# Optimization experiments

Measured on AMD Instinct MI355X. Metric: run time of the kernel, lower is better.

The kernel has to match this reference:

```python
import jax, jax.numpy as jnp
import numpy as np

B, KS, KG, H, V, T = 32, 2048, 512, 512, 32000, 64
BOS = 1


def setup_inputs() -> dict:
    key = jax.random.key(0)
    ks = jax.random.split(key, 11)
    s = 1.0 / np.sqrt(H)
    emb_table = jax.random.normal(ks[4], (V, H), jnp.float32) * s
    emb_table = emb_table.at[0].set(0.0)  # padding_idx=0
    return {
        "sentence_out": jax.random.normal(ks[0], (B, KS, H), jnp.float32),
        "graph_out": jax.random.normal(ks[1], (B, KG, H), jnp.float32),
        "encoder_hidden": jax.random.normal(ks[2], (1, B, H), jnp.float32),
        "W_a": jax.random.normal(ks[3], (H, H), jnp.float32) * s,
        "emb_table": emb_table,
        "W_ih": jax.random.normal(ks[5], (3 * H, H), jnp.float32) * s,
        "W_hh": jax.random.normal(ks[6], (3 * H, H), jnp.float32) * s,
        "b_ih": jnp.zeros((3 * H,), jnp.float32),
        "b_hh": jnp.zeros((3 * H,), jnp.float32),
        "W_out": jax.random.normal(ks[7], (V, 3 * H), jnp.float32) * s,
        "b_out": jnp.zeros((V,), jnp.float32),
        "target_max_length": T,
    }


def _attend(enc, ha, hidden):
    # enc: (B,K,H) values; ha = enc @ W_a: (B,K,H); hidden: (B,H)
    score = jnp.einsum('bkh,bh->bk', ha, hidden)        # (B,K)
    at = jax.nn.softmax(score, axis=1)
    return jnp.einsum('bkh,bk->bh', enc, at)            # (B,H)


def reference(sentence_out, graph_out, encoder_hidden, W_a, emb_table,
              W_ih, W_hh, b_ih, b_hh, W_out, b_out, target_max_length):
    # hoist loop-invariant attention projections
    ha_s = jnp.einsum('bkh,ht->bkt', sentence_out, W_a)  # (B,KS,H)
    ha_g = jnp.einsum('bkh,ht->bkt', graph_out, W_a)     # (B,KG,H)

    def step(carry, _):
        h, inp = carry                                   # h: (B,H), inp: (B,) int
        ct_s = _attend(sentence_out, ha_s, h)
        ct_g = _attend(graph_out, ha_g, h)
        emb = emb_table[inp]                             # (B,H)
        gx = emb @ W_ih.T + b_ih                         # (B,3H)
        gh = h @ W_hh.T + b_hh                           # (B,3H)
        xr, xz, xn = jnp.split(gx, 3, axis=-1)
        hr, hz, hn = jnp.split(gh, 3, axis=-1)
        r = jax.nn.sigmoid(xr + hr)
        z = jax.nn.sigmoid(xz + hz)
        n = jnp.tanh(xn + r * hn)
        h_new = (1.0 - z) * n + z * h                    # (B,H)
        out = jnp.concatenate([h_new, ct_g, ct_s], axis=-1) @ W_out.T + b_out  # (B,V)
        inp_new = jnp.argmax(out, axis=-1)
        return (h_new, inp_new), out

    h0 = encoder_hidden[0]                               # (B,H)
    inp0 = jnp.full((B,), BOS, dtype=jnp.int32)
    _, outs = jax.lax.scan(step, (h0, inp0), None, length=target_max_length)
    return outs                                          # (T,B,V)
```

## Files before the change

### kernel.cpp

```cpp
#include <hip/hip_runtime.h>
#include <hip/hip_bf16.h>
#include <math.h>

#define NB 32
#define NKS 2048
#define NKG 512
#define NH 512
#define NH3 1536
#define NV 32000
#define NSTEPS 64

typedef unsigned long long u64;
typedef unsigned int u32;
typedef unsigned short u16;

__device__ __forceinline__ float bfu(u32 u){ return __uint_as_float(u << 16); }

__device__ __forceinline__ u64 packv(float v, int idx){
  u32 u = __float_as_uint(v);
  u = (u & 0x80000000u) ? ~u : (u | 0x80000000u);
  return (((u64)u) << 32) | (u32)(~(u32)idx);
}

__global__ void k_cast(const float* __restrict__ sent, const float* __restrict__ graph,
                       u16* __restrict__ dsts, u16* __restrict__ dstg){
  const long NSg = (long)NB*NKS*NH/8;
  const long NGg = (long)NB*NKG*NH/8;
  long stride = (long)gridDim.x*blockDim.x;
  for (long g = (long)blockIdx.x*blockDim.x + threadIdx.x; g < NSg+NGg; g += stride){
    const float* src; u16* dst; long gg;
    if (g < NSg){ src = sent; dst = dsts; gg = g; } else { src = graph; dst = dstg; gg = g - NSg; }
    const float4* s4 = (const float4*)src + gg*2;
    float4 a = s4[0], b = s4[1];
    float vals[8] = {a.x,a.y,a.z,a.w,b.x,b.y,b.z,b.w};
    u16 o[8];
    #pragma unroll
    for (int i=0;i<8;i++){
      u32 bits = __float_as_uint(vals[i]);
      o[i] = (u16)((bits + 0x7FFFu + ((bits>>16)&1u)) >> 16);
    }
    uint4 out;
    out.x = (u32)o[0] | ((u32)o[1]<<16);
    out.y = (u32)o[2] | ((u32)o[3]<<16);
    out.z = (u32)o[4] | ((u32)o[5]<<16);
    out.w = (u32)o[6] | ((u32)o[7]<<16);
    *((uint4*)dst + gg) = out;
  }
}

__global__ void k_init(const float* __restrict__ enc, float* __restrict__ h){
  int i = blockIdx.x*256 + threadIdx.x;
  h[i] = enc[i];
}

__global__ __launch_bounds__(512) void k_gates(
    const float* __restrict__ h, const float* __restrict__ Wa,
    const float* __restrict__ Wih, const float* __restrict__ Whh,
    const float* __restrict__ bih, const float* __restrict__ bhh,
    const float* __restrict__ emb, u64* __restrict__ packed,
    float* __restrict__ q, float* __restrict__ gx, float* __restrict__ gh, int step)
{
  __shared__ float4 xs4[NB*128];
  int tid = threadIdx.x;
  int obase = blockIdx.x*64;
  int typ = (obase < NH) ? 0 : (obase < NH+NH3 ? 1 : 2);
  const u64* prev = packed + ((step+1)&1)*NB;
  if (typ != 1){
    for (int i=tid;i<NB*128;i+=512) xs4[i] = ((const float4*)h)[i];
  } else {
    for (int i=tid;i<NB*128;i+=512){
      int b = i>>7;
      int inp = (step==0) ? 1 : (int)(~(u32)prev[b]);
      xs4[i] = ((const float4*)(emb + (size_t)inp*NH))[i&127];
    }
  }
  if (blockIdx.x==0 && tid<NB) packed[(size_t)(step&1)*NB + tid] = 0ULL;
  __syncthreads();
  int lane = tid&63, bg = tid>>6;
  int o = obase + lane;
  const float* wrow; float bias; float* dst; int dstride, dcol;
  if (typ==0){ wrow = Wa + (size_t)o*NH; bias=0.f; dst=q; dstride=NH; dcol=o; }
  else if (typ==1){ int oo=o-NH; wrow = Wih + (size_t)oo*NH; bias=bih[oo]; dst=gx; dstride=NH3; dcol=oo; }
  else { int oo=o-NH-NH3; wrow = Whh + (size_t)oo*NH; bias=bhh[oo]; dst=gh; dstride=NH3; dcol=oo; }
  const float4* w4 = (const float4*)wrow;
  float acc[4] = {0.f,0.f,0.f,0.f};
  for (int k4=0;k4<128;k4++){
    float4 w = w4[k4];
    #pragma unroll
    for (int j=0;j<4;j++){
      float4 xv = xs4[(bg*4+j)*128 + k4];
      acc[j] += w.x*xv.x; acc[j] += w.y*xv.y; acc[j] += w.z*xv.z; acc[j] += w.w*xv.w;
    }
  }
  #pragma unroll
  for (int j=0;j<4;j++){
    int b = bg*4+j;
    dst[(size_t)b*dstride + dcol] = acc[j] + bias;
  }
}

template<int BF>
__global__ __launch_bounds__(256) void k_scores(
   const u16* __restrict__ sh, const u16* __restrict__ g16,
   const float* __restrict__ sf, const float* __restrict__ gf,
   const float* __restrict__ q,
   float* __restrict__ ss, float* __restrict__ sg,
   float* __restrict__ tms, float* __restrict__ tmg)
{
  int blk = blockIdx.x, tid = threadIdx.x;
  int b, tile, K, nt; const u16* srch; const float* srcf; float* sc; float* tm;
  if (blk < 256){ b = blk>>3; tile = blk&7; K = NKS; srch = sh;  srcf = sf; sc = ss; tm = tms; nt=8; }
  else { int bb = blk-256; b = bb>>1; tile = bb&1; K = NKG; srch = g16; srcf = gf; sc = sg; tm = tmg; nt=2; }
  __shared__ float qs[NH];
  for (int i=tid;i<NH;i+=256) qs[i] = q[b*NH+i];
  __syncthreads();
  int key = tile*256 + tid;
  float acc = 0.f;
  if (BF){
    const u16* row = srch + ((size_t)b*K + key)*NH;
    for (int hh=0; hh<NH; hh+=8){
      uint4 u = *(const uint4*)(row+hh);
      acc += bfu(u.x&0xffffu)*qs[hh+0];
      acc += bfu(u.x>>16)    *qs[hh+1];
      acc += bfu(u.y&0xffffu)*qs[hh+2];
      acc += bfu(u.y>>16)    *qs[hh+3];
      acc += bfu(u.z&0xffffu)*qs[hh+4];
      acc += bfu(u.z>>16)    *qs[hh+5];
      acc += bfu(u.w&0xffffu)*qs[hh+6];
      acc += bfu(u.w>>16)    *qs[hh+7];
    }
  } else {
    const float4* row4 = (const float4*)(srcf + ((size_t)b*K + key)*NH);
    for (int k4=0;k4<128;k4++){
      float4 v = row4[k4];
      acc += v.x*qs[k4*4+0]; acc += v.y*qs[k4*4+1]; acc += v.z*qs[k4*4+2]; acc += v.w*qs[k4*4+3];
    }
  }
  sc[(size_t)b*K + key] = acc;
  __shared__ float red[256];
  red[tid] = acc; __syncthreads();
  for (int s=128;s>0;s>>=1){ if (tid<s) red[tid] = fmaxf(red[tid], red[tid+s]); __syncthreads(); }
  if (tid==0) tm[b*nt + tile] = red[0];
}

__global__ __launch_bounds__(256) void k_ct(
  const float* __restrict__ sf, const float* __restrict__ gf,
  const float* __restrict__ q,
  const float* __restrict__ ss, const float* __restrict__ sg,
  const float* __restrict__ tms, const float* __restrict__ tmg,
  float* __restrict__ pcs, float* __restrict__ pcg,
  float* __restrict__ pds, float* __restrict__ pdg)
{
  int blk = blockIdx.x, tid = threadIdx.x;
  int b, tile, K, nt; const float* src; const float* sc; const float* tm; float* pct; float* pden;
  if (blk < 256){ b=blk>>3; tile=blk&7; K=NKS; nt=8; src=sf; sc=ss; tm=tms; pct=pcs; pden=pds; }
  else { int bb=blk-256; b=bb>>1; tile=bb&1; K=NKG; nt=2; src=gf; sc=sg; tm=tmg; pct=pcg; pden=pdg; }
  __shared__ float qs[NH];
  for (int i=tid;i<NH;i+=256) qs[i] = q[b*NH+i];
  float m = -1e30f;
  for (int i=0;i<nt;i++) m = fmaxf(m, tm[b*nt+i]);
  __syncthreads();
  int key = tile*256 + tid;
  float s = sc[(size_t)b*K + key];
  bool selp = (s > m - 24.0f);
  u64 mb = __ballot(selp);
  int lane = tid&63, wv = tid>>6;
  __shared__ int wcnt[4]; __shared__ int wbase[5];
  if (lane==0) wcnt[wv] = __popcll(mb);
  __syncthreads();
  if (tid==0){ int r=0; for (int w=0;w<4;w++){ wbase[w]=r; r+=wcnt[w]; } wbase[4]=r; }
  __syncthreads();
  int n = wbase[4];
  __shared__ int sel[256]; __shared__ float wexp[256];
  if (selp){
    int pos = wbase[wv] + __popcll(mb & ((1ULL<<lane)-1ULL));
    sel[pos] = key;
  }
  __syncthreads();
  for (int i=wv; i<n; i+=4){
    const float* vr = src + ((size_t)b*K + sel[i])*NH;
    const float4* vr4 = (const float4*)vr + lane*2;
    float4 p0 = vr4[0], p1 = vr4[1];
    int hb = lane*8;
    float a = p0.x*qs[hb+0]+p0.y*qs[hb+1]+p0.z*qs[hb+2]+p0.w*qs[hb+3]
            + p1.x*qs[hb+4]+p1.y*qs[hb+5]+p1.z*qs[hb+6]+p1.w*qs[hb+7];
    #pragma unroll
    for (int off=32; off>=1; off>>=1) a += __shfl_xor(a, off);
    if (lane==0) wexp[i] = expf(a - m);
  }
  __syncthreads();
  float den = 0.f;
  for (int i=0;i<n;i++) den += wexp[i];
  float c0=0.f, c1=0.f; int h0 = tid*2;
  for (int i=0;i<n;i++){
    float w = wexp[i];
    const float2 vv = *(const float2*)(src + ((size_t)b*K + sel[i])*NH + h0);
    c0 += w*vv.x; c1 += w*vv.y;
  }
  float* pout = pct + ((size_t)(b*nt + tile))*NH;
  pout[h0] = c0; pout[h0+1] = c1;
  if (tid==0) pden[b*nt+tile] = den;
}

__global__ __launch_bounds__(256) void k_comb(
  const float* __restrict__ pcs, const float* __restrict__ pcg,
  const float* __restrict__ pds, const float* __restrict__ pdg,
  const float* __restrict__ gx, const float* __restrict__ gh,
  float* __restrict__ h, float* __restrict__ x)
{
  int b = blockIdx.x, tid = threadIdx.x;
  float dens = 0.f, deng = 0.f;
  for (int i=0;i<8;i++) dens += pds[b*8+i];
  for (int i=0;i<2;i++) deng += pdg[b*2+i];
  float invs = 1.f/dens, invg = 1.f/deng;
  for (int i=tid; i<NH; i+=256){
    float cs = 0.f; for (int t=0;t<8;t++) cs += pcs[((size_t)(b*8+t))*NH + i];
    float cg = 0.f; for (int t=0;t<2;t++) cg += pcg[((size_t)(b*2+t))*NH + i];
    cs *= invs; cg *= invg;
    float xr = gx[(size_t)b*NH3 + i],        hr = gh[(size_t)b*NH3 + i];
    float xz = gx[(size_t)b*NH3 + NH + i],   hz = gh[(size_t)b*NH3 + NH + i];
    float xn = gx[(size_t)b*NH3 + 2*NH + i], hn = gh[(size_t)b*NH3 + 2*NH + i];
    float r = 1.f/(1.f+expf(-(xr+hr)));
    float z = 1.f/(1.f+expf(-(xz+hz)));
    float nn = tanhf(xn + r*hn);
    float hold = h[(size_t)b*NH + i];
    float hnew = (1.f - z)*nn + z*hold;
    h[(size_t)b*NH + i] = hnew;
    x[(size_t)b*NH3 + i] = hnew;
    x[(size_t)b*NH3 + NH + i] = cg;
    x[(size_t)b*NH3 + 2*NH + i] = cs;
  }
}

__global__ __launch_bounds__(256) void k_logits(
  const float* __restrict__ x, const float* __restrict__ Wout,
  const float* __restrict__ bout, float* __restrict__ dst,
  u64* __restrict__ packed, int step)
{
  __shared__ float4 xs4[NB*128];
  int tid = threadIdx.x;
  int bg = tid>>6, lane = tid&63;
  int vbase = blockIdx.x*128;
  int v0 = vbase + lane, v1 = vbase + 64 + lane;
  float acc0[8] = {0.f,0.f,0.f,0.f,0.f,0.f,0.f,0.f};
  float acc1[8] = {0.f,0.f,0.f,0.f,0.f,0.f,0.f,0.f};
  for (int c=0;c<3;c++){
    int kb = c*NH;
    for (int i=tid;i<NB*128;i+=256){
      int b=i>>7, kk=i&127;
      xs4[i] = ((const float4*)(x + (size_t)b*NH3 + kb))[kk];
    }
    __syncthreads();
    const float4* w0 = (const float4*)(Wout + (size_t)v0*NH3 + kb);
    const float4* w1 = (const float4*)(Wout + (size_t)v1*NH3 + kb);
    for (int k4=0;k4<128;k4++){
      float4 a = w0[k4], bb = w1[k4];
      #pragma unroll
      for (int j=0;j<8;j++){
        float4 xv = xs4[(bg*8+j)*128 + k4];
        acc0[j] += a.x*xv.x;  acc0[j] += a.y*xv.y;  acc0[j] += a.z*xv.z;  acc0[j] += a.w*xv.w;
        acc1[j] += bb.x*xv.x; acc1[j] += bb.y*xv.y; acc1[j] += bb.z*xv.z; acc1[j] += bb.w*xv.w;
      }
    }
    __syncthreads();
  }
  u64* smax = (u64*)xs4;
  if (tid<NB) smax[tid] = 0ULL;
  __syncthreads();
  float b0 = bout[v0], b1 = bout[v1];
  u64* cur = packed + (size_t)(step&1)*NB;
  #pragma unroll
  for (int j=0;j<8;j++){
    int b = bg*8+j;
    float r0 = acc0[j]+b0, r1 = acc1[j]+b1;
    dst[(size_t)b*NV + v0] = r0;
    dst[(size_t)b*NV + v1] = r1;
    u64 p0 = packv(r0, v0), p1 = packv(r1, v1);
    atomicMax(&smax[b], p0>p1?p0:p1);
  }
  __syncthreads();
  if (tid<NB) atomicMax(&cur[tid], smax[tid]);
}

extern "C" void kernel_launch(void* const* d_in, const int* in_sizes, int n_in,
                              void* d_out, int out_size, void* d_ws, size_t ws_size,
                              hipStream_t stream) {
  const float* sent  = (const float*)d_in[0];
  const float* graph = (const float*)d_in[1];
  const float* enc   = (const float*)d_in[2];
  const float* Wa    = (const float*)d_in[3];
  const float* emb   = (const float*)d_in[4];
  const float* Wih   = (const float*)d_in[5];
  const float* Whh   = (const float*)d_in[6];
  const float* bih   = (const float*)d_in[7];
  const float* bhh   = (const float*)d_in[8];
  const float* Wout  = (const float*)d_in[9];
  const float* bout  = (const float*)d_in[10];
  float* out = (float*)d_out;

  char* wsb = (char*)d_ws;
  size_t off = 0;
  auto alloc = [&](size_t nfloats)->float*{ float* p = (float*)(wsb + off); off += nfloats*4; return p; };
  float* h   = alloc(NB*NH);
  float* q   = alloc(NB*NH);
  float* gx  = alloc((size_t)NB*NH3);
  float* gh  = alloc((size_t)NB*NH3);
  float* ss  = alloc((size_t)NB*NKS);
  float* sg  = alloc((size_t)NB*NKG);
  float* tms = alloc(NB*8);
  float* tmg = alloc(NB*2);
  float* pcs = alloc((size_t)NB*8*NH);
  float* pcg = alloc((size_t)NB*2*NH);
  float* pds = alloc(NB*8);
  float* pdg = alloc(NB*2);
  float* x   = alloc((size_t)NB*NH3);
  u64* packed = (u64*)(wsb + off); off += 2*NB*8;
  size_t bfoff = (off + 255) & ~(size_t)255;
  size_t nS = (size_t)NB*NKS*NH, nG = (size_t)NB*NKG*NH;
  int usebf = (ws_size >= bfoff + (nS+nG)*2) ? 1 : 0;
  u16* sh16 = (u16*)(wsb + bfoff);
  u16* g16  = sh16 + nS;

  if (usebf) k_cast<<<dim3(4096), dim3(256), 0, stream>>>(sent, graph, sh16, g16);
  k_init<<<dim3(64), dim3(256), 0, stream>>>(enc, h);

  for (int t=0; t<NSTEPS; t++){
    k_gates<<<dim3(56), dim3(512), 0, stream>>>(h, Wa, Wih, Whh, bih, bhh, emb, packed, q, gx, gh, t);
    if (usebf)
      k_scores<1><<<dim3(320), dim3(256), 0, stream>>>(sh16, g16, sent, graph, q, ss, sg, tms, tmg);
    else
      k_scores<0><<<dim3(320), dim3(256), 0, stream>>>(sh16, g16, sent, graph, q, ss, sg, tms, tmg);
    k_ct<<<dim3(320), dim3(256), 0, stream>>>(sent, graph, q, ss, sg, tms, tmg, pcs, pcg, pds, pdg);
    k_comb<<<dim3(NB), dim3(256), 0, stream>>>(pcs, pcg, pds, pdg, gx, gh, h, x);
    k_logits<<<dim3(250), dim3(256), 0, stream>>>(x, Wout, bout, out + (size_t)t*NB*NV, packed, t);
  }
}
```

Before: 17.49 ms.

## Use bf16 MFMA logits with split-precision activations, fp64 recurrence, and candidate refinement

```diff
diff --git a/kernel.cpp b/kernel.cpp
--- a/kernel.cpp
+++ b/kernel.cpp
@@ -13,13 +13,24 @@
 typedef unsigned long long u64;
 typedef unsigned int u32;
 typedef unsigned short u16;
+typedef __attribute__((ext_vector_type(8))) short short8;
+typedef __attribute__((ext_vector_type(4))) float f32x4;
 
 __device__ __forceinline__ float bfu(u32 u){ return __uint_as_float(u << 16); }
+__device__ __forceinline__ u16 f2bf(float f){
+  u32 b = __float_as_uint(f);
+  return (u16)((b + 0x7FFFu + ((b>>16)&1u)) >> 16);
+}
 
 __device__ __forceinline__ u64 packv(float v, int idx){
   u32 u = __float_as_uint(v);
   u = (u & 0x80000000u) ? ~u : (u | 0x80000000u);
   return (((u64)u) << 32) | (u32)(~(u32)idx);
+}
+__device__ __forceinline__ float unpackv(u64 p){
+  u32 hi = (u32)(p >> 32);
+  u32 u = (hi & 0x80000000u) ? (hi ^ 0x80000000u) : ~hi;
+  return __uint_as_float(u);
 }
 
 __global__ void k_cast(const float* __restrict__ sent, const float* __restrict__ graph,
@@ -35,10 +46,7 @@
     float vals[8] = {a.x,a.y,a.z,a.w,b.x,b.y,b.z,b.w};
     u16 o[8];
     #pragma unroll
-    for (int i=0;i<8;i++){
-      u32 bits = __float_as_uint(vals[i]);
-      o[i] = (u16)((bits + 0x7FFFu + ((bits>>16)&1u)) >> 16);
-    }
+    for (int i=0;i<8;i++) o[i] = f2bf(vals[i]);
     uint4 out;
     out.x = (u32)o[0] | ((u32)o[1]<<16);
     out.y = (u32)o[2] | ((u32)o[3]<<16);
@@ -48,62 +56,90 @@
   }
 }
 
-__global__ void k_init(const float* __restrict__ enc, float* __restrict__ h){
+__global__ void k_packw(const float* __restrict__ W, u16* __restrict__ wp){
+  long t = (long)blockIdx.x*256 + threadIdx.x;
+  int lane = (int)(t & 63);
+  long g = t >> 6;
+  int kc = (int)(g % 48);
+  int v16 = (int)(g / 48);
+  int v = v16*16 + (lane&15);
+  int k0 = kc*32 + (lane>>4)*8;
+  const float4* src = (const float4*)(W + (size_t)v*NH3 + k0);
+  float4 a = src[0], b = src[1];
+  float vals[8] = {a.x,a.y,a.z,a.w,b.x,b.y,b.z,b.w};
+  u16 o[8];
+  #pragma unroll
+  for (int i=0;i<8;i++) o[i] = f2bf(vals[i]);
+  uint4 out;
+  out.x = (u32)o[0] | ((u32)o[1]<<16);
+  out.y = (u32)o[2] | ((u32)o[3]<<16);
+  out.z = (u32)o[4] | ((u32)o[5]<<16);
+  out.w = (u32)o[6] | ((u32)o[7]<<16);
+  ((uint4*)wp)[t] = out;
+}
+
+__global__ void k_init(const float* __restrict__ enc, double* __restrict__ hd){
   int i = blockIdx.x*256 + threadIdx.x;
-  h[i] = enc[i];
-}
-
-__global__ __launch_bounds__(512) void k_gates(
-    const float* __restrict__ h, const float* __restrict__ Wa,
+  hd[i] = (double)enc[i];
+}
+
+__global__ __launch_bounds__(256) void k_gates(
+    const double* __restrict__ hd, const float* __restrict__ Wa,
     const float* __restrict__ Wih, const float* __restrict__ Whh,
     const float* __restrict__ bih, const float* __restrict__ bhh,
-    const float* __restrict__ emb, u64* __restrict__ packed,
-    float* __restrict__ q, float* __restrict__ gx, float* __restrict__ gh, int step)
-{
-  __shared__ float4 xs4[NB*128];
-  int tid = threadIdx.x;
-  int obase = blockIdx.x*64;
-  int typ = (obase < NH) ? 0 : (obase < NH+NH3 ? 1 : 2);
-  const u64* prev = packed + ((step+1)&1)*NB;
+    const float* __restrict__ emb, const u64* __restrict__ packed_ex,
+    double* __restrict__ qd, float* __restrict__ qf,
+    double* __restrict__ gxd, double* __restrict__ ghd, int step)
+{
+  __shared__ double xs[8*512];
+  int blk = blockIdx.x, tid = threadIdx.x;
+  int ot = blk >> 2, bq = blk & 3;
+  int b0 = bq*8;
+  int typ = (ot < 8) ? 0 : (ot < 32 ? 1 : 2);
+  const u64* prev = packed_ex + ((step+1)&1)*NB;
   if (typ != 1){
-    for (int i=tid;i<NB*128;i+=512) xs4[i] = ((const float4*)h)[i];
+    for (int i=tid; i<8*512; i+=256) xs[i] = hd[(size_t)b0*NH + i];
   } else {
-    for (int i=tid;i<NB*128;i+=512){
-      int b = i>>7;
-      int inp = (step==0) ? 1 : (int)(~(u32)prev[b]);
-      xs4[i] = ((const float4*)(emb + (size_t)inp*NH))[i&127];
-    }
-  }
-  if (blockIdx.x==0 && tid<NB) packed[(size_t)(step&1)*NB + tid] = 0ULL;
-  __syncthreads();
-  int lane = tid&63, bg = tid>>6;
-  int o = obase + lane;
-  const float* wrow; float bias; float* dst; int dstride, dcol;
-  if (typ==0){ wrow = Wa + (size_t)o*NH; bias=0.f; dst=q; dstride=NH; dcol=o; }
-  else if (typ==1){ int oo=o-NH; wrow = Wih + (size_t)oo*NH; bias=bih[oo]; dst=gx; dstride=NH3; dcol=oo; }
-  else { int oo=o-NH-NH3; wrow = Whh + (size_t)oo*NH; bias=bhh[oo]; dst=gh; dstride=NH3; dcol=oo; }
+    for (int i=tid; i<8*512; i+=256){
+      int bb = i>>9;
+      int inp = (step==0) ? 1 : (int)(~(u32)prev[b0+bb]);
+      xs[i] = (double)emb[(size_t)inp*NH + (i&511)];
+    }
+  }
+  __syncthreads();
+  int lane = tid&63, wv = tid>>6;
+  const float* wrow; double bias; int dcol;
+  if (typ==0){ dcol = ot*64 + lane; wrow = Wa + (size_t)dcol*NH; bias = 0.0; }
+  else if (typ==1){ dcol = (ot-8)*64 + lane; wrow = Wih + (size_t)dcol*NH; bias = (double)bih[dcol]; }
+  else { dcol = (ot-32)*64 + lane; wrow = Whh + (size_t)dcol*NH; bias = (double)bhh[dcol]; }
   const float4* w4 = (const float4*)wrow;
-  float acc[4] = {0.f,0.f,0.f,0.f};
+  int s0 = wv*2, s1 = s0+1;
+  double acc0 = 0.0, acc1 = 0.0;
   for (int k4=0;k4<128;k4++){
     float4 w = w4[k4];
-    #pragma unroll
-    for (int j=0;j<4;j++){
-      float4 xv = xs4[(bg*4+j)*128 + k4];
-      acc[j] += w.x*xv.x; acc[j] += w.y*xv.y; acc[j] += w.z*xv.z; acc[j] += w.w*xv.w;
-    }
-  }
-  #pragma unroll
-  for (int j=0;j<4;j++){
-    int b = bg*4+j;
-    dst[(size_t)b*dstride + dcol] = acc[j] + bias;
+    int k = k4*4;
+    acc0 += (double)w.x*xs[s0*512+k]   + (double)w.y*xs[s0*512+k+1]
+          + (double)w.z*xs[s0*512+k+2] + (double)w.w*xs[s0*512+k+3];
+    acc1 += (double)w.x*xs[s1*512+k]   + (double)w.y*xs[s1*512+k+1]
+          + (double)w.z*xs[s1*512+k+2] + (double)w.w*xs[s1*512+k+3];
+  }
+  acc0 += bias; acc1 += bias;
+  int ba = b0+s0, bb2 = b0+s1;
+  if (typ==0){
+    qd[(size_t)ba*NH+dcol] = acc0; qf[(size_t)ba*NH+dcol] = (float)acc0;
+    qd[(size_t)bb2*NH+dcol] = acc1; qf[(size_t)bb2*NH+dcol] = (float)acc1;
+  } else if (typ==1){
+    gxd[(size_t)ba*NH3+dcol] = acc0; gxd[(size_t)bb2*NH3+dcol] = acc1;
+  } else {
+    ghd[(size_t)ba*NH3+dcol] = acc0; ghd[(size_t)bb2*NH3+dcol] = acc1;
   }
 }
 
 template<int BF>
-__global__ __launch_bounds__(256) void k_scores(
+__global__ __launch_bounds__(256) void k_scores2(
    const u16* __restrict__ sh, const u16* __restrict__ g16,
    const float* __restrict__ sf, const float* __restrict__ gf,
-   const float* __restrict__ q,
+   const float* __restrict__ qf,
    float* __restrict__ ss, float* __restrict__ sg,
    float* __restrict__ tms, float* __restrict__ tmg)
 {
@@ -111,58 +147,61 @@
   int b, tile, K, nt; const u16* srch; const float* srcf; float* sc; float* tm;
   if (blk < 256){ b = blk>>3; tile = blk&7; K = NKS; srch = sh;  srcf = sf; sc = ss; tm = tms; nt=8; }
   else { int bb = blk-256; b = bb>>1; tile = bb&1; K = NKG; srch = g16; srcf = gf; sc = sg; tm = tmg; nt=2; }
-  __shared__ float qs[NH];
-  for (int i=tid;i<NH;i+=256) qs[i] = q[b*NH+i];
-  __syncthreads();
-  int key = tile*256 + tid;
-  float acc = 0.f;
-  if (BF){
-    const u16* row = srch + ((size_t)b*K + key)*NH;
-    for (int hh=0; hh<NH; hh+=8){
-      uint4 u = *(const uint4*)(row+hh);
-      acc += bfu(u.x&0xffffu)*qs[hh+0];
-      acc += bfu(u.x>>16)    *qs[hh+1];
-      acc += bfu(u.y&0xffffu)*qs[hh+2];
-      acc += bfu(u.y>>16)    *qs[hh+3];
-      acc += bfu(u.z&0xffffu)*qs[hh+4];
-      acc += bfu(u.z>>16)    *qs[hh+5];
-      acc += bfu(u.w&0xffffu)*qs[hh+6];
-      acc += bfu(u.w>>16)    *qs[hh+7];
-    }
-  } else {
-    const float4* row4 = (const float4*)(srcf + ((size_t)b*K + key)*NH);
-    for (int k4=0;k4<128;k4++){
-      float4 v = row4[k4];
-      acc += v.x*qs[k4*4+0]; acc += v.y*qs[k4*4+1]; acc += v.z*qs[k4*4+2]; acc += v.w*qs[k4*4+3];
-    }
-  }
-  sc[(size_t)b*K + key] = acc;
-  __shared__ float red[256];
-  red[tid] = acc; __syncthreads();
-  for (int s=128;s>0;s>>=1){ if (tid<s) red[tid] = fmaxf(red[tid], red[tid+s]); __syncthreads(); }
-  if (tid==0) tm[b*nt + tile] = red[0];
+  int wv = tid>>6, lane = tid&63;
+  float qv[8];
+  { const float4* q4 = (const float4*)(qf + b*NH) + lane*2;
+    float4 qa = q4[0], qb = q4[1];
+    qv[0]=qa.x; qv[1]=qa.y; qv[2]=qa.z; qv[3]=qa.w;
+    qv[4]=qb.x; qv[5]=qb.y; qv[6]=qb.z; qv[7]=qb.w; }
+  int kbase = tile*256 + wv*64;
+  float my = 0.f, wmax = -1e30f;
+  #pragma unroll 2
+  for (int r=0;r<64;r++){
+    int key = kbase + r;
+    float acc;
+    if (BF){
+      uint4 u = *((const uint4*)(srch + ((size_t)b*K + key)*NH) + lane);
+      acc = bfu(u.x&0xffffu)*qv[0]+bfu(u.x>>16)*qv[1]+bfu(u.y&0xffffu)*qv[2]+bfu(u.y>>16)*qv[3]
+           +bfu(u.z&0xffffu)*qv[4]+bfu(u.z>>16)*qv[5]+bfu(u.w&0xffffu)*qv[6]+bfu(u.w>>16)*qv[7];
+    } else {
+      const float4* rw = (const float4*)(srcf + ((size_t)b*K + key)*NH) + lane*2;
+      float4 p0 = rw[0], p1 = rw[1];
+      acc = p0.x*qv[0]+p0.y*qv[1]+p0.z*qv[2]+p0.w*qv[3]
+           +p1.x*qv[4]+p1.y*qv[5]+p1.z*qv[6]+p1.w*qv[7];
+    }
+    #pragma unroll
+    for (int off=32;off>=1;off>>=1) acc += __shfl_xor(acc, off);
+    wmax = fmaxf(wmax, acc);
+    if (r == lane) my = acc;
+  }
+  sc[(size_t)b*K + kbase + lane] = my;
+  __shared__ float red[4];
+  if (lane==0) red[wv] = wmax;
+  __syncthreads();
+  if (tid==0) tm[b*nt + tile] = fmaxf(fmaxf(red[0],red[1]), fmaxf(red[2],red[3]));
 }
 
 __global__ __launch_bounds__(256) void k_ct(
   const float* __restrict__ sf, const float* __restrict__ gf,
-  const float* __restrict__ q,
+  const double* __restrict__ qd,
   const float* __restrict__ ss, const float* __restrict__ sg,
   const float* __restrict__ tms, const float* __restrict__ tmg,
-  float* __restrict__ pcs, float* __restrict__ pcg,
-  float* __restrict__ pds, float* __restrict__ pdg)
+  double* __restrict__ pcs, double* __restrict__ pcg,
+  double* __restrict__ pds, double* __restrict__ pdg)
 {
   int blk = blockIdx.x, tid = threadIdx.x;
-  int b, tile, K, nt; const float* src; const float* sc; const float* tm; float* pct; float* pden;
+  int b, tile, K, nt; const float* src; const float* sc; const float* tm;
+  double* pct; double* pden;
   if (blk < 256){ b=blk>>3; tile=blk&7; K=NKS; nt=8; src=sf; sc=ss; tm=tms; pct=pcs; pden=pds; }
   else { int bb=blk-256; b=bb>>1; tile=bb&1; K=NKG; nt=2; src=gf; sc=sg; tm=tmg; pct=pcg; pden=pdg; }
-  __shared__ float qs[NH];
-  for (int i=tid;i<NH;i+=256) qs[i] = q[b*NH+i];
+  __shared__ double qs[NH];
+  for (int i=tid;i<NH;i+=256) qs[i] = qd[b*NH+i];
   float m = -1e30f;
   for (int i=0;i<nt;i++) m = fmaxf(m, tm[b*nt+i]);
   __syncthreads();
   int key = tile*256 + tid;
   float s = sc[(size_t)b*K + key];
-  bool selp = (s > m - 24.0f);
+  bool selp = (s > m - 30.0f);
   u64 mb = __ballot(selp);
   int lane = tid&63, wv = tid>>6;
   __shared__ int wcnt[4]; __shared__ int wbase[5];
@@ -171,71 +210,190 @@
   if (tid==0){ int r=0; for (int w=0;w<4;w++){ wbase[w]=r; r+=wcnt[w]; } wbase[4]=r; }
   __syncthreads();
   int n = wbase[4];
-  __shared__ int sel[256]; __shared__ float wexp[256];
+  __shared__ int sel[256]; __shared__ double wexp[256];
   if (selp){
     int pos = wbase[wv] + __popcll(mb & ((1ULL<<lane)-1ULL));
     sel[pos] = key;
   }
   __syncthreads();
+  double md = (double)m;
   for (int i=wv; i<n; i+=4){
     const float* vr = src + ((size_t)b*K + sel[i])*NH;
     const float4* vr4 = (const float4*)vr + lane*2;
     float4 p0 = vr4[0], p1 = vr4[1];
     int hb = lane*8;
-    float a = p0.x*qs[hb+0]+p0.y*qs[hb+1]+p0.z*qs[hb+2]+p0.w*qs[hb+3]
-            + p1.x*qs[hb+4]+p1.y*qs[hb+5]+p1.z*qs[hb+6]+p1.w*qs[hb+7];
+    double a = (double)p0.x*qs[hb+0]+(double)p0.y*qs[hb+1]+(double)p0.z*qs[hb+2]+(double)p0.w*qs[hb+3]
+             + (double)p1.x*qs[hb+4]+(double)p1.y*qs[hb+5]+(double)p1.z*qs[hb+6]+(double)p1.w*qs[hb+7];
     #pragma unroll
     for (int off=32; off>=1; off>>=1) a += __shfl_xor(a, off);
-    if (lane==0) wexp[i] = expf(a - m);
-  }
-  __syncthreads();
-  float den = 0.f;
+    if (lane==0) wexp[i] = exp(a - md);
+  }
+  __syncthreads();
+  double den = 0.0;
   for (int i=0;i<n;i++) den += wexp[i];
-  float c0=0.f, c1=0.f; int h0 = tid*2;
+  double c0=0.0, c1=0.0; int h0 = tid*2;
   for (int i=0;i<n;i++){
-    float w = wexp[i];
+    double w = wexp[i];
     const float2 vv = *(const float2*)(src + ((size_t)b*K + sel[i])*NH + h0);
-    c0 += w*vv.x; c1 += w*vv.y;
-  }
-  float* pout = pct + ((size_t)(b*nt + tile))*NH;
+    c0 += w*(double)vv.x; c1 += w*(double)vv.y;
+  }
+  double* pout = pct + ((size_t)(b*nt + tile))*NH;
   pout[h0] = c0; pout[h0+1] = c1;
   if (tid==0) pden[b*nt+tile] = den;
 }
 
 __global__ __launch_bounds__(256) void k_comb(
-  const float* __restrict__ pcs, const float* __restrict__ pcg,
-  const float* __restrict__ pds, const float* __restrict__ pdg,
-  const float* __restrict__ gx, const float* __restrict__ gh,
-  float* __restrict__ h, float* __restrict__ x)
+  const double* __restrict__ pcs, const double* __restrict__ pcg,
+  const double* __restrict__ pds, const double* __restrict__ pdg,
+  const double* __restrict__ gxd, const double* __restrict__ ghd,
+  double* __restrict__ hd, double* __restrict__ xd, u16* __restrict__ apack,
+  u64* __restrict__ pbf_cur, u64* __restrict__ pex_cur)
 {
   int b = blockIdx.x, tid = threadIdx.x;
-  float dens = 0.f, deng = 0.f;
+  if (tid==0){ pbf_cur[b] = 0ULL; pex_cur[b] = 0ULL; }
+  double dens = 0.0, deng = 0.0;
   for (int i=0;i<8;i++) dens += pds[b*8+i];
   for (int i=0;i<2;i++) deng += pdg[b*2+i];
-  float invs = 1.f/dens, invg = 1.f/deng;
+  int mt = b>>4, row = b&15;
   for (int i=tid; i<NH; i+=256){
-    float cs = 0.f; for (int t=0;t<8;t++) cs += pcs[((size_t)(b*8+t))*NH + i];
-    float cg = 0.f; for (int t=0;t<2;t++) cg += pcg[((size_t)(b*2+t))*NH + i];
-    cs *= invs; cg *= invg;
-    float xr = gx[(size_t)b*NH3 + i],        hr = gh[(size_t)b*NH3 + i];
-    float xz = gx[(size_t)b*NH3 + NH + i],   hz = gh[(size_t)b*NH3 + NH + i];
-    float xn = gx[(size_t)b*NH3 + 2*NH + i], hn = gh[(size_t)b*NH3 + 2*NH + i];
-    float r = 1.f/(1.f+expf(-(xr+hr)));
-    float z = 1.f/(1.f+expf(-(xz+hz)));
-    float nn = tanhf(xn + r*hn);
-    float hold = h[(size_t)b*NH + i];
-    float hnew = (1.f - z)*nn + z*hold;
-    h[(size_t)b*NH + i] = hnew;
-    x[(size_t)b*NH3 + i] = hnew;
-    x[(size_t)b*NH3 + NH + i] = cg;
-    x[(size_t)b*NH3 + 2*NH + i] = cs;
+    double cs = 0.0; for (int t=0;t<8;t++) cs += pcs[((size_t)(b*8+t))*NH + i];
+    double cg = 0.0; for (int t=0;t<2;t++) cg += pcg[((size_t)(b*2+t))*NH + i];
+    cs /= dens; cg /= deng;
+    double xr = gxd[(size_t)b*NH3 + i],        hr = ghd[(size_t)b*NH3 + i];
+    double xz = gxd[(size_t)b*NH3 + NH + i],   hz = ghd[(size_t)b*NH3 + NH + i];
+    double xn = gxd[(size_t)b*NH3 + 2*NH + i], hn = ghd[(size_t)b*NH3 + 2*NH + i];
+    double r = 1.0/(1.0+exp(-(xr+hr)));
+    double z = 1.0/(1.0+exp(-(xz+hz)));
+    double nn = tanh(xn + r*hn);
+    double hold = hd[(size_t)b*NH + i];
+    double hnew = (1.0 - z)*nn + z*hold;
+    hd[(size_t)b*NH + i] = hnew;
+    double vals[3] = {hnew, cg, cs};
+    #pragma unroll
+    for (int c=0;c<3;c++){
+      int col = c*NH + i;
+      xd[(size_t)b*NH3 + col] = vals[c];
+      int kc = col>>5, kg = (col&31)>>3, j = col&7;
+      int lane = row + 16*kg;
+      size_t base = ((size_t)(mt*48+kc)*64 + lane)*8 + j;
+      float xf = (float)vals[c];
+      u16 hi = f2bf(xf);
+      float rem = (float)(vals[c] - (double)bfu((u32)hi));
+      apack[base] = hi;
+      apack[base + (size_t)2*48*64*8] = f2bf(rem);
+    }
+  }
+}
+
+__global__ __launch_bounds__(256) void k_logv(
+  const u16* __restrict__ apack, const u16* __restrict__ wpack,
+  const float* __restrict__ bout, float* __restrict__ dst,
+  u64* __restrict__ pbf_cur)
+{
+  int tid = threadIdx.x;
+  int wv = tid>>6, lane = tid&63;
+  int v16 = blockIdx.x*4 + wv;
+  const short8* bp = (const short8*)wpack + (size_t)v16*48*64 + lane;
+  const short8* ap = (const short8*)apack + lane;
+  f32x4 acc0 = {0.f,0.f,0.f,0.f}, acc1 = {0.f,0.f,0.f,0.f};
+  #pragma unroll 4
+  for (int kc=0; kc<48; kc++){
+    short8 bf = bp[(size_t)kc*64];
+    short8 a0h = ap[(size_t)kc*64];
+    short8 a1h = ap[(size_t)(48+kc)*64];
+    short8 a0l = ap[(size_t)(96+kc)*64];
+    short8 a1l = ap[(size_t)(144+kc)*64];
+    acc0 = __builtin_amdgcn_mfma_f32_16x16x32_bf16(a0h, bf, acc0, 0, 0, 0);
+    acc0 = __builtin_amdgcn_mfma_f32_16x16x32_bf16(a0l, bf, acc0, 0, 0, 0);
+    acc1 = __builtin_amdgcn_mfma_f32_16x16x32_bf16(a1h, bf, acc1, 0, 0, 0);
+    acc1 = __builtin_amdgcn_mfma_f32_16x16x32_bf16(a1l, bf, acc1, 0, 0, 0);
+  }
+  __shared__ u64 smax[NB];
+  if (tid < NB) smax[tid] = 0ULL;
+  __syncthreads();
+  int col = v16*16 + (lane&15);
+  float bias = bout[col];
+  int r0 = (lane>>4)*4;
+  #pragma unroll
+  for (int r=0;r<4;r++){
+    int b0 = r0 + r;
+    float v0 = acc0[r] + bias;
+    dst[(size_t)b0*NV + col] = v0;
+    atomicMax(&smax[b0], packv(v0, col));
+    int b1 = 16 + b0;
+    float v1 = acc1[r] + bias;
+    dst[(size_t)b1*NV + col] = v1;
+    atomicMax(&smax[b1], packv(v1, col));
+  }
+  __syncthreads();
+  if (tid < NB) atomicMax(&pbf_cur[tid], smax[tid]);
+}
+
+__global__ __launch_bounds__(256) void k_refine(
+  float* __restrict__ logits, const double* __restrict__ xd,
+  const float* __restrict__ Wout, const float* __restrict__ bout,
+  const u64* __restrict__ pbf_cur, u64* __restrict__ pex_cur)
+{
+  int b = blockIdx.x, tid = threadIdx.x;
+  __shared__ double xs[NH3];
+  for (int i=tid;i<NH3;i+=256) xs[i] = xd[(size_t)b*NH3 + i];
+  float maxv = unpackv(pbf_cur[b]);
+  __shared__ int cnt;
+  __shared__ int cand[2048];
+  __shared__ double cval[2048];
+  const float4* lg = (const float4*)(logits + (size_t)b*NV);
+  float margin = 1.0f;
+  for (int attempt=0; attempt<2; attempt++){
+    if (tid==0) cnt = 0;
+    __syncthreads();
+    float thr = maxv - margin;
+    for (int i=tid; i<NV/4; i+=256){
+      float4 v = lg[i];
+      if (v.x>thr){ int p=atomicAdd(&cnt,1); if(p<2048) cand[p]=i*4+0; }
+      if (v.y>thr){ int p=atomicAdd(&cnt,1); if(p<2048) cand[p]=i*4+1; }
+      if (v.z>thr){ int p=atomicAdd(&cnt,1); if(p<2048) cand[p]=i*4+2; }
+      if (v.w>thr){ int p=atomicAdd(&cnt,1); if(p<2048) cand[p]=i*4+3; }
+    }
+    __syncthreads();
+    if (cnt <= 2048) break;
+    margin = 0.125f;
+    __syncthreads();
+  }
+  int n = min(cnt, 2048);
+  int wv = tid>>6, lane = tid&63;
+  for (int c=wv; c<n; c+=4){
+    int v = cand[c];
+    const float4* wr = (const float4*)(Wout + (size_t)v*NH3);
+    double a = 0.0;
+    #pragma unroll
+    for (int i=0;i<6;i++){
+      int e = lane + 64*i;
+      float4 w4 = wr[e];
+      a += (double)w4.x*xs[e*4+0] + (double)w4.y*xs[e*4+1]
+         + (double)w4.z*xs[e*4+2] + (double)w4.w*xs[e*4+3];
+    }
+    #pragma unroll
+    for (int off=32; off>=1; off>>=1) a += __shfl_xor(a, off);
+    if (lane==0){
+      double av = a + (double)bout[v];
+      cval[c] = av;
+      logits[(size_t)b*NV + v] = (float)av;
+    }
+  }
+  __syncthreads();
+  if (tid==0){
+    double bv = -1e300; int bi = 0x7fffffff;
+    for (int c=0;c<n;c++){
+      if (cval[c] > bv || (cval[c] == bv && cand[c] < bi)){ bv = cval[c]; bi = cand[c]; }
+    }
+    pex_cur[b] = packv((float)bv, bi);
   }
 }
 
 __global__ __launch_bounds__(256) void k_logits(
-  const float* __restrict__ x, const float* __restrict__ Wout,
+  const double* __restrict__ xd, const float* __restrict__ Wout,
   const float* __restrict__ bout, float* __restrict__ dst,
-  u64* __restrict__ packed, int step)
+  u64* __restrict__ pbf_cur)
 {
   __shared__ float4 xs4[NB*128];
   int tid = threadIdx.x;
@@ -248,7 +406,12 @@
     int kb = c*NH;
     for (int i=tid;i<NB*128;i+=256){
       int b=i>>7, kk=i&127;
-      xs4[i] = ((const float4*)(x + (size_t)b*NH3 + kb))[kk];
+      float4 t;
+      t.x = (float)xd[(size_t)b*NH3 + kb + kk*4+0];
+      t.y = (float)xd[(size_t)b*NH3 + kb + kk*4+1];
+      t.z = (float)xd[(size_t)b*NH3 + kb + kk*4+2];
+      t.w = (float)xd[(size_t)b*NH3 + kb + kk*4+3];
+      xs4[i] = t;
     }
     __syncthreads();
     const float4* w0 = (const float4*)(Wout + (size_t)v0*NH3 + kb);
@@ -268,7 +431,6 @@
   if (tid<NB) smax[tid] = 0ULL;
   __syncthreads();
   float b0 = bout[v0], b1 = bout[v1];
-  u64* cur = packed + (size_t)(step&1)*NB;
   #pragma unroll
   for (int j=0;j<8;j++){
     int b = bg*8+j;
@@ -279,7 +441,7 @@
     atomicMax(&smax[b], p0>p1?p0:p1);
   }
   __syncthreads();
-  if (tid<NB) atomicMax(&cur[tid], smax[tid]);
+  if (tid<NB) atomicMax(&pbf_cur[tid], smax[tid]);
 }
 
 extern "C" void kernel_launch(void* const* d_in, const int* in_sizes, int n_in,
@@ -300,38 +462,59 @@
 
   char* wsb = (char*)d_ws;
   size_t off = 0;
-  auto alloc = [&](size_t nfloats)->float*{ float* p = (float*)(wsb + off); off += nfloats*4; return p; };
-  float* h   = alloc(NB*NH);
-  float* q   = alloc(NB*NH);
-  float* gx  = alloc((size_t)NB*NH3);
-  float* gh  = alloc((size_t)NB*NH3);
-  float* ss  = alloc((size_t)NB*NKS);
-  float* sg  = alloc((size_t)NB*NKG);
-  float* tms = alloc(NB*8);
-  float* tmg = alloc(NB*2);
-  float* pcs = alloc((size_t)NB*8*NH);
-  float* pcg = alloc((size_t)NB*2*NH);
-  float* pds = alloc(NB*8);
-  float* pdg = alloc(NB*2);
-  float* x   = alloc((size_t)NB*NH3);
-  u64* packed = (u64*)(wsb + off); off += 2*NB*8;
-  size_t bfoff = (off + 255) & ~(size_t)255;
+  auto allocd = [&](size_t n)->double*{ double* p = (double*)(wsb + off); off += n*8; return p; };
+  auto allocf = [&](size_t n)->float*{ float* p = (float*)(wsb + off); off += n*4; return p; };
+  double* hd  = allocd(NB*NH);
+  double* qd  = allocd(NB*NH);
+  float*  qf  = allocf(NB*NH);
+  double* gxd = allocd((size_t)NB*NH3);
+  double* ghd = allocd((size_t)NB*NH3);
+  double* xd  = allocd((size_t)NB*NH3);
+  double* pcs = allocd((size_t)NB*8*NH);
+  double* pcg = allocd((size_t)NB*2*NH);
+  double* pds = allocd(NB*8);
+  double* pdg = allocd(NB*2);
+  float* ss  = allocf((size_t)NB*NKS);
+  float* sg  = allocf((size_t)NB*NKG);
+  float* tms = allocf(NB*8);
+  float* tmg = allocf(NB*2);
+  u64* packed_bf = (u64*)(wsb + off); off += 2*NB*8;
+  u64* packed_ex = (u64*)(wsb + off); off += 2*NB*8;
+  u16* apack = (u16*)(wsb + off); off += (size_t)4*48*64*8*2;
+
+  size_t wpoff = (off + 255) & ~(size_t)255;
+  const size_t WPBYTES = (size_t)2000*48*64*16;
+  int usew = (ws_size >= wpoff + WPBYTES) ? 1 : 0;
+  u16* wpack = (u16*)(wsb + wpoff);
+
+  size_t bfoff = usew ? ((wpoff + WPBYTES + 255) & ~(size_t)255) : wpoff;
   size_t nS = (size_t)NB*NKS*NH, nG = (size_t)NB*NKG*NH;
   int usebf = (ws_size >= bfoff + (nS+nG)*2) ? 1 : 0;
   u16* sh16 = (u16*)(wsb + bfoff);
   u16* g16  = sh16 + nS;
 
+  if (usew) k_packw<<<dim3(24000), dim3(256), 0, stream>>>(Wout, wpack);
   if (usebf) k_cast<<<dim3(4096), dim3(256), 0, stream>>>(sent, graph, sh16, g16);
-  k_init<<<dim3(64), dim3(256), 0, stream>>>(enc, h);
+  k_init<<<dim3(64), dim3(256), 0, stream>>>(enc, hd);
 
   for (int t=0; t<NSTEPS; t++){
-    k_gates<<<dim3(56), dim3(512), 0, stream>>>(h, Wa, Wih, Whh, bih, bhh, emb, packed, q, gx, gh, t);
+    int cur = t&1;
+    u64* pbf_cur = packed_bf + (size_t)cur*NB;
+    u64* pex_cur = packed_ex + (size_t)cur*NB;
+    k_gates<<<dim3(224), dim3(256), 0, stream>>>(hd, Wa, Wih, Whh, bih, bhh, emb,
+                                                 packed_ex, qd, qf, gxd, ghd, t);
     if (usebf)
-      k_scores<1><<<dim3(320), dim3(256), 0, stream>>>(sh16, g16, sent, graph, q, ss, sg, tms, tmg);
+      k_scores2<1><<<dim3(320), dim3(256), 0, stream>>>(sh16, g16, sent, graph, qf, ss, sg, tms, tmg);
     else
-      k_scores<0><<<dim3(320), dim3(256), 0, stream>>>(sh16, g16, sent, graph, q, ss, sg, tms, tmg);
-    k_ct<<<dim3(320), dim3(256), 0, stream>>>(sent, graph, q, ss, sg, tms, tmg, pcs, pcg, pds, pdg);
-    k_comb<<<dim3(NB), dim3(256), 0, stream>>>(pcs, pcg, pds, pdg, gx, gh, h, x);
-    k_logits<<<dim3(250), dim3(256), 0, stream>>>(x, Wout, bout, out + (size_t)t*NB*NV, packed, t);
-  }
-}
+      k_scores2<0><<<dim3(320), dim3(256), 0, stream>>>(sh16, g16, sent, graph, qf, ss, sg, tms, tmg);
+    k_ct<<<dim3(320), dim3(256), 0, stream>>>(sent, graph, qd, ss, sg, tms, tmg, pcs, pcg, pds, pdg);
+    k_comb<<<dim3(NB), dim3(256), 0, stream>>>(pcs, pcg, pds, pdg, gxd, ghd, hd, xd, apack, pbf_cur, pex_cur);
+    float* dst = out + (size_t)t*NB*NV;
+    if (usew){
+      k_logv<<<dim3(500), dim3(256), 0, stream>>>(apack, wpack, bout, dst, pbf_cur);
+    } else {
+      k_logits<<<dim3(250), dim3(256), 0, stream>>>(xd, Wout, bout, dst, pbf_cur);
+    }
+    k_refine<<<dim3(NB), dim3(256), 0, stream>>>(dst, xd, Wout, bout, pbf_cur, pex_cur);
+  }
+}
```

Measured after the change: 30.51 ms. 1.74x slower.
